# Kernel optimization log

Measured on AMD Instinct MI355X. Metric: run time of the kernel, lower is better.

The kernel has to match this reference:

```python
import jax, jax.numpy as jnp
import numpy as np

KH = KW = 3
STRIDE = 1
ITERATIONS = 2
EPS = 1e-7


def _squash(s):
    # squash along last axis (capsule dim)
    sn = jnp.sum(s * s, axis=-1, keepdims=True)
    return (sn / (1.0 + sn)) * s / jnp.sqrt(sn + EPS)


def setup_inputs() -> dict:
    key = jax.random.key(0)
    k1, k2 = jax.random.split(key)
    x = jax.random.normal(k1, (4, 14, 14, 32, 8), dtype=jnp.float32)
    # W: [1,1,1,filters_out, caps_per_patch=3*3*32, dims_out=16, dims_in=8], stddev=0.1 init
    W = 0.1 * jax.random.normal(k2, (1, 1, 1, 32, 288, 16, 8), dtype=jnp.float32)
    return {"x": x, "W": W}


def reference(x, W):
    B, H, Wd, Fin, Din = x.shape
    Ho = (H - KH) // STRIDE + 1
    Wo = (Wd - KW) // STRIDE + 1
    # Patch extraction, channel order (kh, kw, Fin) to match tf.image.extract_patches
    patches = jnp.stack(
        [x[:, i:i + Ho * STRIDE:STRIDE, j:j + Wo * STRIDE:STRIDE]
         for i in range(KH) for j in range(KW)],
        axis=3,
    )  # [B,Ho,Wo,KH*KW,Fin,Din]
    patches = patches.reshape(B, Ho, Wo, KH * KW * Fin, Din)  # [B,Ho,Wo,C,Di]

    Wm = W[0, 0, 0]  # [F, C, Do, Di]
    F, C, Do, _ = Wm.shape
    # predictions[b,h,w,f,c,o] = sum_i W[f,c,o,i] * patches[b,h,w,c,i]
    preds = jnp.einsum('fcoi,bhwci->bhwfco', Wm, patches)

    logits = jnp.zeros((B, Ho, Wo, F, C), dtype=preds.dtype)
    outputs = jnp.zeros((B, Ho, Wo, F, Do), dtype=preds.dtype)
    for _ in range(ITERATIONS):
        # agreement = predictions^T @ outputs over the dims_out axis
        agreement = jnp.einsum('bhwfco,bhwfo->bhwfc', preds, outputs)
        logits = logits + agreement
        # NOTE: original code softmaxes over axis=3 (the filters_out axis)
        cc = jax.nn.softmax(logits, axis=3)  # [B,Ho,Wo,F,C]
        centroids = jnp.sum(cc[..., None] * preds, axis=4)  # [B,Ho,Wo,F,Do]
        outputs = _squash(centroids)
    return outputs
```

## Files before the change

kernel.cpp:

```cpp
#include <hip/hip_runtime.h>

#define NB   4
#define H_IN 14
#define W_IN 14
#define FIN  32
#define DI   8
#define F    32
#define C    288
#define DO   16
#define HO   12
#define WO   12
#define NPOS (NB*HO*WO)
#define EPS  1e-7f

#define CH   16
#define CC   (C/CH)
#define GP   2
#define GRID2 ((CH*NPOS/GP)/4)

#define KTOT  (C*DI)
#define KHALF 1152
#define KPADH 1156

#define W2H_BYTES  ((size_t)F*C*DO*DI*2)
#define WH_BYTES   ((size_t)F*C*DO*DI*2)
#define PH_BYTES   ((size_t)NPOS*KTOT*2)
#define PART_BYTES ((size_t)CH*NPOS*F*DO*4)
#define OUT1P_BYTES ((size_t)2*NPOS*F*DO*4)

#define CVT_W2H 576
#define CVT_WH  576
#define CVT_PH  648
#define CVT_GRID (CVT_W2H + CVT_WH + CVT_PH)

typedef _Float16 h2 __attribute__((ext_vector_type(2)));
typedef _Float16 h8v __attribute__((ext_vector_type(8)));
typedef float    f4v __attribute__((ext_vector_type(4)));

__device__ __forceinline__ unsigned int pack2(float a, float b) {
    h2 v; v.x = (_Float16)a; v.y = (_Float16)b;
    return __builtin_bit_cast(unsigned int, v);
}

__device__ __forceinline__ float dot8h(const uint4 w, const uint4 v, float acc) {
#if __has_builtin(__builtin_amdgcn_fdot2)
    acc = __builtin_amdgcn_fdot2(__builtin_bit_cast(h2, w.x), __builtin_bit_cast(h2, v.x), acc, false);
    acc = __builtin_amdgcn_fdot2(__builtin_bit_cast(h2, w.y), __builtin_bit_cast(h2, v.y), acc, false);
    acc = __builtin_amdgcn_fdot2(__builtin_bit_cast(h2, w.z), __builtin_bit_cast(h2, v.z), acc, false);
    acc = __builtin_amdgcn_fdot2(__builtin_bit_cast(h2, w.w), __builtin_bit_cast(h2, v.w), acc, false);
#else
    const h2 w0 = __builtin_bit_cast(h2, w.x), v0 = __builtin_bit_cast(h2, v.x);
    const h2 w1 = __builtin_bit_cast(h2, w.y), v1 = __builtin_bit_cast(h2, v.y);
    const h2 w2 = __builtin_bit_cast(h2, w.z), v2 = __builtin_bit_cast(h2, v.z);
    const h2 w3 = __builtin_bit_cast(h2, w.w), v3 = __builtin_bit_cast(h2, v.w);
    acc += (float)w0.x*(float)v0.x + (float)w0.y*(float)v0.y
         + (float)w1.x*(float)v1.x + (float)w1.y*(float)v1.y
         + (float)w2.x*(float)v2.x + (float)w2.y*(float)v2.y
         + (float)w3.x*(float)v3.x + (float)w3.y*(float)v3.y;
#endif
    return acc;
}

__device__ __forceinline__ int xbase_of(int pos) {
    const int b = pos/(HO*WO), rem = pos%(HO*WO), ho = rem/WO, wo = rem%WO;
    return ((b*H_IN + ho)*W_IN + wo)*FIN*DI;
}

__device__ __forceinline__ int coff_of(int c) {
    const int slab = c >> 5, fin = c & 31;
    const int kh = slab/3, kw = slab%3;
    return (kh*W_IN + kw)*FIN*DI + fin*DI;
}

__global__ __launch_bounds__(256) void kernConv(const float* __restrict__ Wt,
                                                const float* __restrict__ x,
                                                unsigned short* __restrict__ W2h,
                                                unsigned short* __restrict__ Wh,
                                                unsigned short* __restrict__ Ph) {
    const int b = blockIdx.x;
    if (b < CVT_W2H) {
        const int idx = b*256 + threadIdx.x;
        const float* src = Wt + (size_t)idx*8;
        const float4 a = *(const float4*)src;
        const float4 bb = *(const float4*)(src + 4);
        uint4 r;
        r.x = pack2(a.x, a.y);   r.y = pack2(a.z, a.w);
        r.z = pack2(bb.x, bb.y); r.w = pack2(bb.z, bb.w);
        const int o = idx & 15;
        const int c = (idx >> 4) % C;
        const int f = idx / (C*DO);
        ((uint4*)W2h)[(size_t)(c*DO + o)*F + f] = r;
    } else if (b < CVT_W2H + CVT_WH) {
        const int idx = (b - CVT_W2H)*256 + threadIdx.x;
        const float* src = Wt + (size_t)idx*8;
        const float4 a = *(const float4*)src;
        const float4 bb = *(const float4*)(src + 4);
        uint4 r;
        r.x = pack2(a.x, a.y);   r.y = pack2(a.z, a.w);
        r.z = pack2(bb.x, bb.y); r.w = pack2(bb.z, bb.w);
        ((uint4*)Wh)[idx] = r;
    } else {
        const int pc = (b - CVT_W2H - CVT_WH)*256 + threadIdx.x;
        const int pos = pc / C, c = pc % C;
        const float* src = x + xbase_of(pos) + coff_of(c);
        const float4 a = *(const float4*)src;
        const float4 bb = *(const float4*)(src + 4);
        uint4 r;
        r.x = pack2(a.x, a.y);   r.y = pack2(a.z, a.w);
        r.z = pack2(bb.x, bb.y); r.w = pack2(bb.z, bb.w);
        ((uint4*)Ph)[pc] = r;
    }
}

__global__ __launch_bounds__(256) void kernM1(const unsigned short* __restrict__ Ph,
                                              const unsigned short* __restrict__ Wh,
                                              float* __restrict__ out1p)
{
    __shared__ unsigned short As[16][KPADH];

    const int tid  = threadIdx.x;
    const int lane = tid & 63;
    const int wv   = tid >> 6;
    const int ks   = blockIdx.x & 1;
    const int fg   = (blockIdx.x >> 1) & 7;
    const int pt   = blockIdx.x >> 4;
    const int f    = wv*8 + fg;
    const int pos0 = pt*16;
    const int n    = lane & 15, q = lane >> 4;

    #pragma unroll
    for (int r = 0; r < 9; ++r) {
        const int linear = r*256 + tid;
        const int row = linear / 144, col = linear % 144;
        const uint4 v = *(const uint4*)(Ph + (size_t)(pos0 + row)*KTOT + ks*KHALF + col*8);
        *(uint4*)&As[row][col*8] = v;
    }
    __syncthreads();

    const unsigned short* pa = &As[n][q*8];
    const unsigned short* pb = Wh + ((size_t)(f*C + ks*144 + q)*DO + n)*DI;

    f4v acc0 = {0.f,0.f,0.f,0.f}, acc1 = {0.f,0.f,0.f,0.f};
    #pragma unroll 4
    for (int s = 0; s < 36; s += 2) {
        const h8v a0 = *(const h8v*)(pa + s*32);
        const h8v b0 = *(const h8v*)(pb + (size_t)s*4*DO*DI);
        const h8v a1 = *(const h8v*)(pa + (s+1)*32);
        const h8v b1 = *(const h8v*)(pb + (size_t)(s+1)*4*DO*DI);
        acc0 = __builtin_amdgcn_mfma_f32_16x16x32_f16(a0, b0, acc0, 0, 0, 0);
        acc1 = __builtin_amdgcn_mfma_f32_16x16x32_f16(a1, b1, acc1, 0, 0, 0);
    }

    #pragma unroll
    for (int r = 0; r < 4; ++r) {
        out1p[((size_t)ks*NPOS + pos0 + q*4 + r)*512 + f*DO + n] = acc0[r] + acc1[r];
    }
}

__global__ __launch_bounds__(256) void kern2w(const unsigned short* __restrict__ Ph,
                                              const unsigned short* __restrict__ W2h,
                                              const float* __restrict__ out1p,
                                              float* __restrict__ part2)
{
    const int tid  = threadIdx.x;
    const int lane = tid & 63;
    const int wv   = tid >> 6;
    const int f    = lane & 31;
    const int og   = lane >> 5;
    const int o0   = og*8;

    const int ch   = blockIdx.x & (CH-1);
    const int gq   = blockIdx.x >> 4;
    const int grp  = __builtin_amdgcn_readfirstlane(gq*4 + wv);
    const int pos0 = grp*GP;

    const int c0 = ch*CC;
    const uint4* W2h4 = (const uint4*)W2h;

    float u[8][GP];
    #pragma unroll
    for (int p = 0; p < GP; ++p) {
        const float* up0 = out1p + (size_t)(pos0 + p)*512 + f*DO + o0;
        const float* up1 = up0 + (size_t)NPOS*512;
        const float4 a0 = *(const float4*)up0;
        const float4 b0 = *(const float4*)(up0 + 4);
        const float4 a1 = *(const float4*)up1;
        const float4 b1 = *(const float4*)(up1 + 4);
        float ur[8];
        ur[0]=(a0.x+a1.x)*(1.f/32.f); ur[1]=(a0.y+a1.y)*(1.f/32.f);
        ur[2]=(a0.z+a1.z)*(1.f/32.f); ur[3]=(a0.w+a1.w)*(1.f/32.f);
        ur[4]=(b0.x+b1.x)*(1.f/32.f); ur[5]=(b0.y+b1.y)*(1.f/32.f);
        ur[6]=(b0.z+b1.z)*(1.f/32.f); ur[7]=(b0.w+b1.w)*(1.f/32.f);
        float sq = 0.f;
        #pragma unroll
        for (int k = 0; k < 8; ++k) sq += ur[k]*ur[k];
        sq += __shfl_xor(sq, 32);
        const float sc = (sq/(1.f + sq)) * rsqrtf(sq + EPS);
        #pragma unroll
        for (int k = 0; k < 8; ++k) u[k][p] = ur[k]*sc;
    }

    float acc[8][GP];
    #pragma unroll
    for (int k = 0; k < 8; ++k)
        #pragma unroll
        for (int p = 0; p < GP; ++p) acc[k][p] = 0.f;

    #pragma unroll 1
    for (int cl = 0; cl < CC; ++cl) {
        const int c = c0 + cl;

        uint4 xv[GP];
        #pragma unroll
        for (int p = 0; p < GP; ++p)
            xv[p] = *(const uint4*)(Ph + (size_t)(pos0 + p)*KTOT + c*DI);

        float pred[8][GP];
        #pragma unroll
        for (int k = 0; k < 8; ++k) {
            const uint4 w = W2h4[(size_t)(c*DO + o0 + k)*F + f];
            #pragma unroll
            for (int p = 0; p < GP; ++p) pred[k][p] = dot8h(w, xv[p], 0.f);
        }

        #pragma unroll
        for (int p = 0; p < GP; ++p) {
            float ap = 0.f;
            #pragma unroll
            for (int k = 0; k < 8; ++k) ap += pred[k][p]*u[k][p];
            ap += __shfl_xor(ap, 32);

            const float e = __expf(ap);
            float s = e;
            s += __shfl_xor(s, 1);
            s += __shfl_xor(s, 2);
            s += __shfl_xor(s, 4);
            s += __shfl_xor(s, 8);
            s += __shfl_xor(s, 16);
            const float cc = e / s;

            #pragma unroll
            for (int k = 0; k < 8; ++k) acc[k][p] += cc*pred[k][p];
        }
    }

    #pragma unroll
    for (int p = 0; p < GP; ++p) {
        float* dst = part2 + ((size_t)(ch*NPOS + pos0 + p)*F + f)*DO + o0;
        float4 s0, s1;
        s0.x=acc[0][p]; s0.y=acc[1][p]; s0.z=acc[2][p]; s0.w=acc[3][p];
        s1.x=acc[4][p]; s1.y=acc[5][p]; s1.z=acc[6][p]; s1.w=acc[7][p];
        *(float4*)dst = s0;
        *(float4*)(dst + 4) = s1;
    }
}

__global__ __launch_bounds__(64) void kern3(const float* __restrict__ part2,
                                            float* __restrict__ out)
{
    const int lane = threadIdx.x;
    const int pos  = blockIdx.x;
    const int f = lane & 31, oh = lane >> 5, o0 = oh*8;

    float c0x=0.f,c0y=0.f,c0z=0.f,c0w=0.f, c1x=0.f,c1y=0.f,c1z=0.f,c1w=0.f;
    #pragma unroll
    for (int k = 0; k < CH; ++k) {
        const float* s = part2 + ((size_t)(k*NPOS + pos)*F + f)*DO + o0;
        const float4 a = *(const float4*)s;
        const float4 b = *(const float4*)(s + 4);
        c0x+=a.x; c0y+=a.y; c0z+=a.z; c0w+=a.w;
        c1x+=b.x; c1y+=b.y; c1z+=b.z; c1w+=b.w;
    }
    float sq = c0x*c0x + c0y*c0y + c0z*c0z + c0w*c0w
             + c1x*c1x + c1y*c1y + c1z*c1z + c1w*c1w;
    sq += __shfl_xor(sq, 32);
    const float sc = (sq/(1.f + sq)) * rsqrtf(sq + EPS);

    float* dst = out + ((size_t)pos*F + f)*DO + o0;
    float4 s0, s1;
    s0.x=c0x*sc; s0.y=c0y*sc; s0.z=c0z*sc; s0.w=c0w*sc;
    s1.x=c1x*sc; s1.y=c1y*sc; s1.z=c1z*sc; s1.w=c1w*sc;
    *(float4*)dst = s0;
    *(float4*)(dst + 4) = s1;
}

__device__ __forceinline__ float dot8(const float4* __restrict__ w,
                                      const float4 p0, const float4 p1) {
    float4 a = w[0], b = w[1];
    return a.x*p0.x + a.y*p0.y + a.z*p0.z + a.w*p0.w
         + b.x*p1.x + b.y*p1.y + b.z*p1.z + b.w*p1.w;
}

__global__ __launch_bounds__(256) void capsule_kernel_f32(
    const float* __restrict__ x, const float* __restrict__ Wt,
    float* __restrict__ out)
{
    __shared__ float patch[C*DI];
    __shared__ float cent[F*DO];
    __shared__ float out1[F*DO];
    __shared__ float agr[F*C];
    __shared__ float scale_s[F];

    const int tid = threadIdx.x;
    const int pos = blockIdx.x;
    const int b   = pos / (HO*WO);
    const int rem = pos % (HO*WO);
    const int ho  = rem / WO;
    const int wo  = rem % WO;

    #pragma unroll
    for (int slab = 0; slab < 9; ++slab) {
        const int kh = slab / 3, kw = slab % 3;
        const float* src = x + (((b*H_IN + ho + kh)*W_IN + (wo + kw))*FIN)*DI;
        patch[slab*256 + tid] = src[tid];
    }
    __syncthreads();

    const float4* pv = (const float4*)patch;

    {
        const int fo0 = tid, fo1 = tid + 256;
        const int f0 = fo0 >> 4, o0 = fo0 & 15;
        const int f1 = fo1 >> 4, o1 = fo1 & 15;
        float acc0 = 0.f, acc1 = 0.f;
        for (int c = 0; c < C; ++c) {
            const float4 p0 = pv[c*2], p1 = pv[c*2+1];
            acc0 += dot8((const float4*)(Wt + ((f0*C + c)*DO + o0)*DI), p0, p1);
            acc1 += dot8((const float4*)(Wt + ((f1*C + c)*DO + o1)*DI), p0, p1);
        }
        cent[fo0] = acc0 * (1.f/32.f);
        cent[fo1] = acc1 * (1.f/32.f);
    }
    __syncthreads();

    if (tid < F) {
        float sn = 0.f;
        #pragma unroll
        for (int o = 0; o < DO; ++o) { float v = cent[tid*DO + o]; sn += v*v; }
        const float sc = (sn/(1.f + sn)) * rsqrtf(sn + EPS);
        #pragma unroll
        for (int o = 0; o < DO; ++o) out1[tid*DO + o] = cent[tid*DO + o] * sc;
    }
    __syncthreads();

    #pragma unroll 1
    for (int r = 0; r < (F*C)/256; ++r) {
        const int pp = tid + 256*r;
        const int f = pp / C, c = pp % C;
        const float4* wrow = (const float4*)(Wt + (f*C + c)*DO*DI);
        const float4 p0 = pv[c*2], p1 = pv[c*2+1];
        float a = 0.f;
        #pragma unroll
        for (int o = 0; o < DO; ++o) a += dot8(wrow + o*2, p0, p1) * out1[f*DO + o];
        agr[pp] = a;
    }
    __syncthreads();

    for (int c = tid; c < C; c += 256) {
        float m = -1e30f;
        #pragma unroll
        for (int f = 0; f < F; ++f) m = fmaxf(m, agr[f*C + c]);
        float s = 0.f;
        #pragma unroll
        for (int f = 0; f < F; ++f) {
            const float e = __expf(agr[f*C + c] - m);
            agr[f*C + c] = e; s += e;
        }
        const float inv = 1.f / s;
        #pragma unroll
        for (int f = 0; f < F; ++f) agr[f*C + c] *= inv;
    }
    __syncthreads();

    {
        const int fo0 = tid, fo1 = tid + 256;
        const int f0 = fo0 >> 4, o0 = fo0 & 15;
        const int f1 = fo1 >> 4, o1 = fo1 & 15;
        float acc0 = 0.f, acc1 = 0.f;
        for (int c = 0; c < C; ++c) {
            const float4 p0 = pv[c*2], p1 = pv[c*2+1];
            acc0 += agr[f0*C + c] * dot8((const float4*)(Wt + ((f0*C + c)*DO + o0)*DI), p0, p1);
            acc1 += agr[f1*C + c] * dot8((const float4*)(Wt + ((f1*C + c)*DO + o1)*DI), p0, p1);
        }
        cent[fo0] = acc0;
        cent[fo1] = acc1;
    }
    __syncthreads();

    if (tid < F) {
        float sn = 0.f;
        #pragma unroll
        for (int o = 0; o < DO; ++o) { float v = cent[tid*DO + o]; sn += v*v; }
        scale_s[tid] = (sn/(1.f + sn)) * rsqrtf(sn + EPS);
    }
    __syncthreads();

    out[pos*(F*DO) + tid]       = cent[tid]       * scale_s[tid >> 4];
    out[pos*(F*DO) + tid + 256] = cent[tid + 256] * scale_s[(tid >> 4) + 16];
}

extern "C" void kernel_launch(void* const* d_in, const int* in_sizes, int n_in,
                              void* d_out, int out_size, void* d_ws, size_t ws_size,
                              hipStream_t stream) {
    const float* x  = (const float*)d_in[0];
    const float* Wt = (const float*)d_in[1];
    float* out = (float*)d_out;

    if (ws_size >= W2H_BYTES + WH_BYTES + PH_BYTES + PART_BYTES + OUT1P_BYTES) {
        char* p = (char*)d_ws;
        unsigned short* W2h = (unsigned short*)p;            p += W2H_BYTES;
        unsigned short* Wh  = (unsigned short*)p;            p += WH_BYTES;
        unsigned short* Ph  = (unsigned short*)p;            p += PH_BYTES;
        float* part = (float*)p;                             p += PART_BYTES;
        float* out1p = (float*)p;

        kernConv<<<CVT_GRID, 256, 0, stream>>>(Wt, x, W2h, Wh, Ph);
        kernM1<<<36*8*2, 256, 0, stream>>>(Ph, Wh, out1p);
        kern2w<<<GRID2, 256, 0, stream>>>(Ph, W2h, out1p, part);
        kern3<<<NPOS, 64, 0, stream>>>(part, out);
    } else {
        capsule_kernel_f32<<<NPOS, 256, 0, stream>>>(x, Wt, out);
    }
}
```

Before: 124.5 us.

## Split capsule axis into 32 chunks and parallelize final reduction across 256 threads

Doubles the number of capsule chunks in the routing kernel so it launches twice as many blocks, each covering half as many capsules. This raises parallelism in the main kernel. The cost is twice the partial-sum traffic into the final kernel. To absorb that, the final reduction kernel now runs 256 threads per position: two halves each sum half of the chunks with float4 loads, combine through shared memory, and reduce the squash norm with shuffles across groups of four lanes. The workspace for partial sums grows, and the size check on the workspace could now send execution to the fallback path if the buffer is too small.

```diff
diff --git a/kernel.cpp b/kernel.cpp
--- a/kernel.cpp
+++ b/kernel.cpp
@@ -13,7 +13,7 @@
 #define NPOS (NB*HO*WO)
 #define EPS  1e-7f
 
-#define CH   16
+#define CH   32
 #define CC   (C/CH)
 #define GP   2
 #define GRID2 ((CH*NPOS/GP)/4)
@@ -170,7 +170,7 @@
     const int o0   = og*8;
 
     const int ch   = blockIdx.x & (CH-1);
-    const int gq   = blockIdx.x >> 4;
+    const int gq   = blockIdx.x >> 5;
     const int grp  = __builtin_amdgcn_readfirstlane(gq*4 + wv);
     const int pos0 = grp*GP;
 
@@ -255,33 +255,38 @@
     }
 }
 
-__global__ __launch_bounds__(64) void kern3(const float* __restrict__ part2,
-                                            float* __restrict__ out)
+__global__ __launch_bounds__(256) void kern3(const float* __restrict__ part2,
+                                             float* __restrict__ out)
 {
-    const int lane = threadIdx.x;
+    __shared__ float4 red[128];
+
+    const int tid  = threadIdx.x;
     const int pos  = blockIdx.x;
-    const int f = lane & 31, oh = lane >> 5, o0 = oh*8;
-
-    float c0x=0.f,c0y=0.f,c0z=0.f,c0w=0.f, c1x=0.f,c1y=0.f,c1z=0.f,c1w=0.f;
-    #pragma unroll
-    for (int k = 0; k < CH; ++k) {
-        const float* s = part2 + ((size_t)(k*NPOS + pos)*F + f)*DO + o0;
-        const float4 a = *(const float4*)s;
-        const float4 b = *(const float4*)(s + 4);
-        c0x+=a.x; c0y+=a.y; c0z+=a.z; c0w+=a.w;
-        c1x+=b.x; c1y+=b.y; c1z+=b.z; c1w+=b.w;
-    }
-    float sq = c0x*c0x + c0y*c0y + c0z*c0z + c0w*c0w
-             + c1x*c1x + c1y*c1y + c1z*c1z + c1w*c1w;
-    sq += __shfl_xor(sq, 32);
-    const float sc = (sq/(1.f + sq)) * rsqrtf(sq + EPS);
-
-    float* dst = out + ((size_t)pos*F + f)*DO + o0;
-    float4 s0, s1;
-    s0.x=c0x*sc; s0.y=c0y*sc; s0.z=c0z*sc; s0.w=c0w*sc;
-    s1.x=c1x*sc; s1.y=c1y*sc; s1.z=c1z*sc; s1.w=c1w*sc;
-    *(float4*)dst = s0;
-    *(float4*)(dst + 4) = s1;
+    const int half = tid >> 7;
+    const int slot = tid & 127;
+    const int f = slot >> 2, q = slot & 3;
+
+    float ax=0.f, ay=0.f, az=0.f, aw=0.f;
+    #pragma unroll 4
+    for (int k = 0; k < CH/2; ++k) {
+        const int kk = half*(CH/2) + k;
+        const float4 v = *(const float4*)(part2 + ((size_t)(kk*NPOS + pos)*F + f)*DO + q*4);
+        ax += v.x; ay += v.y; az += v.z; aw += v.w;
+    }
+    if (half) { float4 r; r.x=ax; r.y=ay; r.z=az; r.w=aw; red[slot] = r; }
+    __syncthreads();
+    if (!half) {
+        const float4 o = red[slot];
+        ax += o.x; ay += o.y; az += o.z; aw += o.w;
+
+        float sq = ax*ax + ay*ay + az*az + aw*aw;
+        sq += __shfl_xor(sq, 1);
+        sq += __shfl_xor(sq, 2);
+        const float sc = (sq/(1.f + sq)) * rsqrtf(sq + EPS);
+
+        float4 s; s.x=ax*sc; s.y=ay*sc; s.z=az*sc; s.w=aw*sc;
+        *(float4*)(out + ((size_t)pos*F + f)*DO + q*4) = s;
+    }
 }
 
 __device__ __forceinline__ float dot8(const float4* __restrict__ w,
@@ -417,7 +422,7 @@
         kernConv<<<CVT_GRID, 256, 0, stream>>>(Wt, x, W2h, Wh, Ph);
         kernM1<<<36*8*2, 256, 0, stream>>>(Ph, Wh, out1p);
         kern2w<<<GRID2, 256, 0, stream>>>(Ph, W2h, out1p, part);
-        kern3<<<NPOS, 64, 0, stream>>>(part, out);
+        kern3<<<NPOS, 256, 0, stream>>>(part, out);
     } else {
         capsule_kernel_f32<<<NPOS, 256, 0, stream>>>(x, Wt, out);
     }
```

New measurement: 123.8 us. No clear change (-0.6%).
